# Kernel tuning notes

Measured on AMD Instinct MI355X. Metric: run time of the kernel, lower is better.

The kernel has to match this reference:

```python
import jax, jax.numpy as jnp
import numpy as np

N, E, H = 50000, 800000, 128
EPS = 1e-5

def _init(key, shape, fan_in):
    return jax.random.normal(key, shape, dtype=jnp.float32) / np.sqrt(fan_in)

def setup_inputs() -> dict:
    key = jax.random.key(0)
    ks = jax.random.split(key, 20)
    x = jax.random.normal(ks[0], (N, 3), dtype=jnp.float32)
    h = jax.random.normal(ks[1], (N, H), dtype=jnp.float32)
    edge_index = jax.random.randint(ks[2], (2, E), 0, N, dtype=jnp.int32)
    d_ei = 2 * H + 1
    return {
        "x": x, "h": h, "edge_index": edge_index,
        "We1": _init(ks[3], (d_ei, H), d_ei), "be1": jnp.zeros((H,), jnp.float32),
        "We2": _init(ks[4], (H, H), H),       "be2": jnp.zeros((H,), jnp.float32),
        "Wc1": _init(ks[5], (H, H), H),       "bc1": jnp.zeros((H,), jnp.float32),
        "Wc2": _init(ks[6], (H, 1), H),       "bc2": jnp.zeros((1,), jnp.float32),
        "Wn1": _init(ks[7], (2 * H, H), 2 * H), "bn1": jnp.zeros((H,), jnp.float32),
        "Wn2": _init(ks[8], (H, H), H),       "bn2": jnp.zeros((H,), jnp.float32),
        "gamma": jnp.ones((H,), jnp.float32), "beta": jnp.zeros((H,), jnp.float32),
    }

def reference(x, h, edge_index, We1, be1, We2, be2, Wc1, bc1, Wc2, bc2,
              Wn1, bn1, Wn2, bn2, gamma, beta):
    act = jax.nn.silu
    row, col = edge_index[0], edge_index[1]
    n = x.shape[0]
    rel = x[row] - x[col]                                  # [E,3]
    dist2 = jnp.sum(rel * rel, axis=-1, keepdims=True)     # [E,1]
    edge_input = jnp.concatenate([h[row], h[col], dist2], axis=-1)  # [E,2H+1]
    ef = act(edge_input @ We1 + be1)
    ef = act(ef @ We2 + be2)                                # [E,H]
    gate = act(ef @ Wc1 + bc1) @ Wc2 + bc2                  # [E,1]
    # scatter-mean by row (shared counts for coords and features)
    counts = jax.ops.segment_sum(jnp.ones((rel.shape[0], 1), x.dtype), row, num_segments=n)
    counts = jnp.clip(counts, 1.0)
    dx = jax.ops.segment_sum(rel * gate, row, num_segments=n) / counts
    x_out = x + dx
    agg = jax.ops.segment_sum(ef, row, num_segments=n) / counts     # [N,H]
    dh = act(jnp.concatenate([h, agg], axis=-1) @ Wn1 + bn1) @ Wn2 + bn2
    h2 = h + dh
    mu = jnp.mean(h2, axis=-1, keepdims=True)
    var = jnp.mean((h2 - mu) ** 2, axis=-1, keepdims=True)
    h_norm = (h2 - mu) / jnp.sqrt(var + EPS) * gamma + beta
    h_out = act(h_norm)
    return x_out, h_out
```

## Files before the change

kernel.cpp:

```cpp
#include <hip/hip_runtime.h>

#define NN 50000
#define NE 800000
#define HD 128

typedef __attribute__((ext_vector_type(4))) float vf32x4;
typedef __attribute__((ext_vector_type(8))) __bf16 vbf16x8;
typedef __attribute__((ext_vector_type(4))) unsigned short vushort4;
typedef __attribute__((ext_vector_type(8))) unsigned short vushort8;

constexpr size_t OFF_AGG   = 0;
constexpr size_t OFF_DX    = 25600000;
constexpr size_t OFF_HIST  = 26200000;
constexpr size_t OFF_CUR   = 26400000;
constexpr size_t ZBYTES    = 26600000;
constexpr size_t OFF_START = 26600000;
constexpr size_t OFF_PERM  = 26800704;
constexpr size_t OFF_HBF   = 30000704;
constexpr size_t OFF_HR    = 42800704;
constexpr size_t OFF_HC    = 55600704;
constexpr size_t OFF_WE1P  = 68400704;
constexpr size_t OFF_WE2P  = OFF_WE1P + 65536;
constexpr size_t OFF_WC1P  = OFF_WE2P + 32768;
constexpr size_t OFF_WN1P  = OFF_WC1P + 32768;
constexpr size_t OFF_WN2P  = OFF_WN1P + 65536;

__device__ __forceinline__ unsigned short f2bf(float f) {
    unsigned int u = __float_as_uint(f);
    u += 0x7fffu + ((u >> 16) & 1u);
    return (unsigned short)(u >> 16);
}

__device__ __forceinline__ float bf2f(unsigned short b) {
    return __uint_as_float((unsigned int)b << 16);
}

__device__ __forceinline__ float silu(float v) {
    return __fdividef(v, 1.0f + __expf(-v));
}

__global__ __launch_bounds__(256) void h2bf_kernel(const float* __restrict__ h,
                                                   unsigned short* __restrict__ h_bf) {
    int idx = blockIdx.x * 256 + threadIdx.x;
    vf32x4 v = ((const vf32x4*)h)[idx];
    vushort4 o;
    o[0] = f2bf(v[0]); o[1] = f2bf(v[1]); o[2] = f2bf(v[2]); o[3] = f2bf(v[3]);
    ((vushort4*)h_bf)[idx] = o;
}

__device__ __forceinline__ void pack_one(const float* __restrict__ src,
                                         unsigned short* __restrict__ dst,
                                         int local, int KB) {
    int j = local & 7;
    int lane = (local >> 3) & 63;
    int rest = local >> 9;
    int kb = rest % KB;
    int t = rest / KB;
    int srow = kb * 32 + ((lane >> 4) << 3) + j;
    int scol = t * 16 + (lane & 15);
    dst[local] = f2bf(src[srow * 128 + scol]);
}

__global__ __launch_bounds__(256) void pack_w_kernel(
    const float* __restrict__ We1, const float* __restrict__ We2,
    const float* __restrict__ Wc1, const float* __restrict__ Wn1,
    const float* __restrict__ Wn2,
    unsigned short* __restrict__ We1p, unsigned short* __restrict__ We2p,
    unsigned short* __restrict__ Wc1p, unsigned short* __restrict__ Wn1p,
    unsigned short* __restrict__ Wn2p) {
    int idx = blockIdx.x * 256 + threadIdx.x;
    if (idx < 32768)       pack_one(We1, We1p, idx, 8);
    else if (idx < 49152)  pack_one(We2, We2p, idx - 32768, 4);
    else if (idx < 65536)  pack_one(Wc1, Wc1p, idx - 49152, 4);
    else if (idx < 98304)  pack_one(Wn1, Wn1p, idx - 65536, 8);
    else                   pack_one(Wn2, Wn2p, idx - 98304, 4);
}

__global__ __launch_bounds__(256) void hist_kernel(const int* __restrict__ ei,
                                                   int* __restrict__ hist) {
    int e = blockIdx.x * 256 + threadIdx.x;
    atomicAdd(&hist[ei[e]], 1);
}

#define SCAN_T 1024
#define SCAN_C 49
__global__ __launch_bounds__(1024) void scan_kernel(const int* __restrict__ hist,
                                                    int* __restrict__ row_start) {
    __shared__ int part[SCAN_T];
    int t = threadIdx.x;
    int base = t * SCAN_C;
    int s = 0;
#pragma unroll
    for (int j = 0; j < SCAN_C; j++) {
        int idx = base + j;
        if (idx < NN) s += hist[idx];
    }
    part[t] = s;
    __syncthreads();
    for (int off = 1; off < SCAN_T; off <<= 1) {
        int v = (t >= off) ? part[t - off] : 0;
        __syncthreads();
        part[t] += v;
        __syncthreads();
    }
    int run = (t == 0) ? 0 : part[t - 1];
    for (int j = 0; j < SCAN_C; j++) {
        int idx = base + j;
        if (idx < NN) {
            row_start[idx] = run;
            run += hist[idx];
        }
    }
}

__global__ __launch_bounds__(256) void scatter_kernel(const int* __restrict__ ei,
                                                      const int* __restrict__ row_start,
                                                      int* __restrict__ cursor,
                                                      int* __restrict__ perm) {
    int e = blockIdx.x * 256 + threadIdx.x;
    int r = ei[e];
    int pos = row_start[r] + atomicAdd(&cursor[r], 1);
    perm[pos] = e;
}

__global__ __launch_bounds__(256, 4) void hprep_kernel(
    const unsigned short* __restrict__ h_bf,
    const unsigned short* __restrict__ We1p,
    unsigned short* __restrict__ hr, unsigned short* __restrict__ hc) {
    const int tid = threadIdx.x;
    const int nbase = blockIdx.x * 64;
    const int wave = tid >> 6, lane = tid & 63;
    const int li = lane & 15, grp = lane >> 4;

    int mynode = nbase + wave * 16 + li;
    if (mynode >= NN) mynode = NN - 1;

    vbf16x8 af[4];
    const unsigned short* ph = h_bf + (size_t)mynode * 128 + grp * 8;
#pragma unroll
    for (int kb = 0; kb < 4; kb++) af[kb] = *(const vbf16x8*)(ph + kb * 32);

    const vf32x4 vzero = {0.f, 0.f, 0.f, 0.f};
    vf32x4 ar[8], ac[8];
#pragma unroll
    for (int t = 0; t < 8; t++) { ar[t] = vzero; ac[t] = vzero; }
#pragma unroll
    for (int kb = 0; kb < 4; kb++) {
#pragma unroll
        for (int t = 0; t < 8; t++) {
            vbf16x8 br = *(const vbf16x8*)(We1p + ((t * 8 + kb) * 64 + lane) * 8);
            ar[t] = __builtin_amdgcn_mfma_f32_16x16x32_bf16(af[kb], br, ar[t], 0, 0, 0);
            vbf16x8 bc_ = *(const vbf16x8*)(We1p + ((t * 8 + 4 + kb) * 64 + lane) * 8);
            ac[t] = __builtin_amdgcn_mfma_f32_16x16x32_bf16(af[kb], bc_, ac[t], 0, 0, 0);
        }
    }
#pragma unroll
    for (int t = 0; t < 8; t++) {
        int col = t * 16 + li;
#pragma unroll
        for (int r = 0; r < 4; r++) {
            int node = nbase + wave * 16 + grp * 4 + r;
            if (node < NN) {
                hr[(size_t)node * 128 + col] = f2bf(ar[t][r]);
                hc[(size_t)node * 128 + col] = f2bf(ac[t][r]);
            }
        }
    }
}

__global__ __launch_bounds__(256, 4) void edge_kernel(
    const float* __restrict__ x, const int* __restrict__ ei,
    const int* __restrict__ perm,
    const unsigned short* __restrict__ hr, const unsigned short* __restrict__ hc,
    const unsigned short* __restrict__ We2p, const unsigned short* __restrict__ Wc1p,
    const float* __restrict__ We1, const float* __restrict__ be1,
    const float* __restrict__ be2, const float* __restrict__ bc1,
    const float* __restrict__ Wc2, const float* __restrict__ bc2,
    float* __restrict__ dxsum, float* __restrict__ agg) {

    __shared__ __align__(16) unsigned short s_ef[64 * 136];
    __shared__ float s_rel[64 * 4];
    __shared__ int s_row[64];
    __shared__ int s_col[64];

    const int tid = threadIdx.x;
    const int ebase = blockIdx.x * 64;

    if (tid < 64) {
        int e = perm[ebase + tid];
        int r = ei[e], c = ei[NE + e];
        s_row[tid] = r;
        s_col[tid] = c;
        float d0 = x[r * 3 + 0] - x[c * 3 + 0];
        float d1 = x[r * 3 + 1] - x[c * 3 + 1];
        float d2v = x[r * 3 + 2] - x[c * 3 + 2];
        s_rel[tid * 4 + 0] = d0;
        s_rel[tid * 4 + 1] = d1;
        s_rel[tid * 4 + 2] = d2v;
        s_rel[tid * 4 + 3] = d0 * d0 + d1 * d1 + d2v * d2v;
    }
    __syncthreads();

    const int wave = tid >> 6, lane = tid & 63;
    const int li = lane & 15, grp = lane >> 4;
    const int el = wave * 16 + li;
    const vf32x4 vzero = {0.f, 0.f, 0.f, 0.f};

    vbf16x8 af[4];
    {
        const unsigned short* pr = hr + (size_t)s_row[el] * 128 + grp * 8;
        const unsigned short* pc = hc + (size_t)s_col[el] * 128 + grp * 8;
        const float d2e = s_rel[el * 4 + 3];
        const float* wlast = We1 + 256 * 128;
#pragma unroll
        for (int kb = 0; kb < 4; kb++) {
            vushort8 ua = *(const vushort8*)(pr + kb * 32);
            vushort8 ub = *(const vushort8*)(pc + kb * 32);
            int cbase = kb * 32 + grp * 8;
            vushort8 o;
#pragma unroll
            for (int j = 0; j < 8; j++) {
                float v = bf2f(ua[j]) + bf2f(ub[j]) + d2e * wlast[cbase + j] + be1[cbase + j];
                o[j] = f2bf(silu(v));
            }
            af[kb] = *(vbf16x8*)&o;
        }
    }

    vf32x4 acc[8];
#pragma unroll
    for (int t = 0; t < 8; t++) acc[t] = vzero;
#pragma unroll
    for (int kb = 0; kb < 4; kb++) {
#pragma unroll
        for (int t = 0; t < 8; t++) {
            vbf16x8 b = *(const vbf16x8*)(We2p + ((t * 4 + kb) * 64 + lane) * 8);
            acc[t] = __builtin_amdgcn_mfma_f32_16x16x32_bf16(af[kb], b, acc[t], 0, 0, 0);
        }
    }
#pragma unroll
    for (int t = 0; t < 8; t++) {
        int col = t * 16 + li;
        float b2 = be2[col];
#pragma unroll
        for (int r = 0; r < 4; r++)
            s_ef[(wave * 16 + grp * 4 + r) * 136 + col] = f2bf(silu(acc[t][r] + b2));
    }
    __syncthreads();

#pragma unroll
    for (int t = 0; t < 8; t++) acc[t] = vzero;
    {
        const unsigned short* arow = s_ef + (wave * 16 + li) * 136 + grp * 8;
#pragma unroll
        for (int kb = 0; kb < 4; kb++) {
            vbf16x8 a = *(const vbf16x8*)(arow + kb * 32);
#pragma unroll
            for (int t = 0; t < 8; t++) {
                vbf16x8 b = *(const vbf16x8*)(Wc1p + ((t * 4 + kb) * 64 + lane) * 8);
                acc[t] = __builtin_amdgcn_mfma_f32_16x16x32_bf16(a, b, acc[t], 0, 0, 0);
            }
        }
    }
    float gp[4] = {0.f, 0.f, 0.f, 0.f};
#pragma unroll
    for (int t = 0; t < 8; t++) {
        int col = t * 16 + li;
        float bc = bc1[col], w2 = Wc2[col];
#pragma unroll
        for (int r = 0; r < 4; r++) gp[r] += silu(acc[t][r] + bc) * w2;
    }
#pragma unroll
    for (int r = 0; r < 4; r++) {
#pragma unroll
        for (int d = 1; d < 16; d <<= 1) gp[r] += __shfl_xor(gp[r], d, 16);
        gp[r] += bc2[0];
    }

#pragma unroll
    for (int r = 0; r < 4; r++) {
        int e2 = wave * 16 + grp * 4 + r;
        int node = s_row[e2];
        if (li < 3)
            atomicAdd(&dxsum[node * 3 + li], s_rel[e2 * 4 + li] * gp[r]);
    }

    {
        int col = tid & 127;
        int half = tid >> 7;
        int ebeg = half * 32;
        float acc2 = 0.f;
        int cur = s_row[ebeg];
#pragma unroll 4
        for (int e = ebeg; e < ebeg + 32; ++e) {
            int rr = s_row[e];
            float v = bf2f(s_ef[e * 136 + col]);
            if (rr != cur) {
                atomicAdd(&agg[(size_t)cur * 128 + col], acc2);
                acc2 = 0.f;
                cur = rr;
            }
            acc2 += v;
        }
        atomicAdd(&agg[(size_t)cur * 128 + col], acc2);
    }
}

__global__ __launch_bounds__(256, 4) void node_kernel(
    const float* __restrict__ x, const float* __restrict__ h32,
    const unsigned short* __restrict__ h_bf,
    const int* __restrict__ hist, const float* __restrict__ dxsum,
    const float* __restrict__ agg,
    const unsigned short* __restrict__ Wn1p, const unsigned short* __restrict__ Wn2p,
    const float* __restrict__ bn1, const float* __restrict__ bn2,
    const float* __restrict__ gamma, const float* __restrict__ beta,
    float* __restrict__ out) {

    __shared__ __align__(16) unsigned short s_agg[64 * 136];
    __shared__ __align__(16) unsigned short s_ef[64 * 136];

    const int tid = threadIdx.x;
    const int nbase = blockIdx.x * 64;

    {
        int idx = blockIdx.x * 192 + tid;
        if (tid < 192 && idx < NN * 3) {
            int node = idx / 3;
            float cnt = fmaxf((float)hist[node], 1.0f);
            out[idx] = x[idx] + dxsum[idx] / cnt;
        }
    }
#pragma unroll
    for (int i = 0; i < 8; i++) {
        int flat = i * 256 + tid;
        int row = flat >> 5, q = flat & 31;
        int node = nbase + row;
        if (node >= NN) node = NN - 1;
        float inv = 1.0f / fmaxf((float)hist[node], 1.0f);
        vf32x4 v = *(const vf32x4*)(agg + (size_t)node * 128 + q * 4);
        vushort4 o;
        o[0] = f2bf(v[0] * inv); o[1] = f2bf(v[1] * inv);
        o[2] = f2bf(v[2] * inv); o[3] = f2bf(v[3] * inv);
        *(vushort4*)(&s_agg[row * 136 + q * 4]) = o;
    }
    __syncthreads();

    const int wave = tid >> 6, lane = tid & 63;
    const int li = lane & 15, grp = lane >> 4;
    const vf32x4 vzero = {0.f, 0.f, 0.f, 0.f};

    int mynode = nbase + wave * 16 + li;
    if (mynode >= NN) mynode = NN - 1;

    vbf16x8 af[8];
    {
        const unsigned short* ph = h_bf + (size_t)mynode * 128 + grp * 8;
#pragma unroll
        for (int kb = 0; kb < 4; kb++) af[kb] = *(const vbf16x8*)(ph + kb * 32);
        const unsigned short* pa = s_agg + (wave * 16 + li) * 136 + grp * 8;
#pragma unroll
        for (int kb = 0; kb < 4; kb++) af[4 + kb] = *(const vbf16x8*)(pa + kb * 32);
    }
    vf32x4 acc[8];
#pragma unroll
    for (int t = 0; t < 8; t++) acc[t] = vzero;
#pragma unroll
    for (int kb = 0; kb < 8; kb++) {
#pragma unroll
        for (int t = 0; t < 8; t++) {
            vbf16x8 b = *(const vbf16x8*)(Wn1p + ((t * 8 + kb) * 64 + lane) * 8);
            acc[t] = __builtin_amdgcn_mfma_f32_16x16x32_bf16(af[kb], b, acc[t], 0, 0, 0);
        }
    }
#pragma unroll
    for (int t = 0; t < 8; t++) {
        int col = t * 16 + li;
        float b1 = bn1[col];
#pragma unroll
        for (int r = 0; r < 4; r++) {
            float v = silu(acc[t][r] + b1);
            s_ef[(wave * 16 + grp * 4 + r) * 136 + col] = f2bf(v);
        }
    }
    __syncthreads();

#pragma unroll
    for (int t = 0; t < 8; t++) acc[t] = vzero;
    {
        const unsigned short* arow = s_ef + (wave * 16 + li) * 136 + grp * 8;
#pragma unroll
        for (int kb = 0; kb < 4; kb++) {
            vbf16x8 a = *(const vbf16x8*)(arow + kb * 32);
#pragma unroll
            for (int t = 0; t < 8; t++) {
                vbf16x8 b = *(const vbf16x8*)(Wn2p + ((t * 4 + kb) * 64 + lane) * 8);
                acc[t] = __builtin_amdgcn_mfma_f32_16x16x32_bf16(a, b, acc[t], 0, 0, 0);
            }
        }
    }
    float h2v[8][4];
    float sum[4] = {0.f, 0.f, 0.f, 0.f}, sq[4] = {0.f, 0.f, 0.f, 0.f};
#pragma unroll
    for (int t = 0; t < 8; t++) {
        int col = t * 16 + li;
        float b2 = bn2[col];
#pragma unroll
        for (int r = 0; r < 4; r++) {
            int node = nbase + wave * 16 + grp * 4 + r;
            int nc = node < NN ? node : NN - 1;
            float v = acc[t][r] + b2 + h32[(size_t)nc * 128 + col];
            h2v[t][r] = v;
            sum[r] += v;
            sq[r] += v * v;
        }
    }
    float mu[4], rstd[4];
#pragma unroll
    for (int r = 0; r < 4; r++) {
#pragma unroll
        for (int d = 1; d < 16; d <<= 1) {
            sum[r] += __shfl_xor(sum[r], d, 16);
            sq[r] += __shfl_xor(sq[r], d, 16);
        }
        mu[r] = sum[r] * (1.0f / 128.0f);
        float var = sq[r] * (1.0f / 128.0f) - mu[r] * mu[r];
        rstd[r] = rsqrtf(var + 1e-5f);
    }
#pragma unroll
    for (int t = 0; t < 8; t++) {
        int col = t * 16 + li;
        float g = gamma[col], bt = beta[col];
#pragma unroll
        for (int r = 0; r < 4; r++) {
            int node = nbase + wave * 16 + grp * 4 + r;
            if (node < NN) {
                float vn = (h2v[t][r] - mu[r]) * rstd[r] * g + bt;
                out[NN * 3 + (size_t)node * 128 + col] = silu(vn);
            }
        }
    }
}

extern "C" void kernel_launch(void* const* d_in, const int* in_sizes, int n_in,
                              void* d_out, int out_size, void* d_ws, size_t ws_size,
                              hipStream_t stream) {
    const float* x     = (const float*)d_in[0];
    const float* h     = (const float*)d_in[1];
    const int* ei      = (const int*)d_in[2];
    const float* We1   = (const float*)d_in[3];
    const float* be1   = (const float*)d_in[4];
    const float* We2   = (const float*)d_in[5];
    const float* be2   = (const float*)d_in[6];
    const float* Wc1   = (const float*)d_in[7];
    const float* bc1   = (const float*)d_in[8];
    const float* Wc2   = (const float*)d_in[9];
    const float* bc2   = (const float*)d_in[10];
    const float* Wn1   = (const float*)d_in[11];
    const float* bn1   = (const float*)d_in[12];
    const float* Wn2   = (const float*)d_in[13];
    const float* bn2   = (const float*)d_in[14];
    const float* gamma = (const float*)d_in[15];
    const float* beta  = (const float*)d_in[16];
    float* out = (float*)d_out;

    char* ws = (char*)d_ws;
    float* agg            = (float*)(ws + OFF_AGG);
    float* dxsum          = (float*)(ws + OFF_DX);
    int* hist             = (int*)(ws + OFF_HIST);
    int* cursor           = (int*)(ws + OFF_CUR);
    int* row_start        = (int*)(ws + OFF_START);
    int* perm             = (int*)(ws + OFF_PERM);
    unsigned short* h_bf  = (unsigned short*)(ws + OFF_HBF);
    unsigned short* hr_bf = (unsigned short*)(ws + OFF_HR);
    unsigned short* hc_bf = (unsigned short*)(ws + OFF_HC);
    unsigned short* We1p  = (unsigned short*)(ws + OFF_WE1P);
    unsigned short* We2p  = (unsigned short*)(ws + OFF_WE2P);
    unsigned short* Wc1p  = (unsigned short*)(ws + OFF_WC1P);
    unsigned short* Wn1p  = (unsigned short*)(ws + OFF_WN1P);
    unsigned short* Wn2p  = (unsigned short*)(ws + OFF_WN2P);

    hipMemsetAsync(ws, 0, ZBYTES, stream);
    h2bf_kernel<<<NN * 128 / 4 / 256, 256, 0, stream>>>(h, h_bf);
    pack_w_kernel<<<114688 / 256, 256, 0, stream>>>(We1, We2, Wc1, Wn1, Wn2,
                                                    We1p, We2p, Wc1p, Wn1p, Wn2p);
    hist_kernel<<<NE / 256, 256, 0, stream>>>(ei, hist);
    scan_kernel<<<1, SCAN_T, 0, stream>>>(hist, row_start);
    scatter_kernel<<<NE / 256, 256, 0, stream>>>(ei, row_start, cursor, perm);
    hprep_kernel<<<(NN + 63) / 64, 256, 0, stream>>>(h_bf, We1p, hr_bf, hc_bf);
    edge_kernel<<<NE / 64, 256, 0, stream>>>(x, ei, perm, hr_bf, hc_bf, We2p, Wc1p,
                                             We1, be1, be2, bc1, Wc2, bc2,
                                             dxsum, agg);
    node_kernel<<<(NN + 63) / 64, 256, 0, stream>>>(x, h, h_bf, hist, dxsum, agg,
                                                    Wn1p, Wn2p, bn1, bn2, gamma, beta, out);
}
```

Before: 607.6 us.

## Parallelize row scan, fuse bf16 conversion into hprep, tune edge kernel

Replaces the single-block serial prefix scan with a three-kernel multi-block scan (block sums, scan of sums, local scan plus offset). Folds the h to bf16 conversion into hprep so one kernel launch and a pass over h disappear. In the edge kernel it caches the last We1 row and be1 in shared memory, raises the launch-bounds occupancy hint to 8 blocks per SM, and changes the segmented aggregation to two columns per thread over 16-edge chunks. The higher occupancy hint may force register spills, and the shorter chunks may issue more atomics.

```diff
diff --git a/kernel.cpp b/kernel.cpp
--- a/kernel.cpp
+++ b/kernel.cpp
@@ -24,6 +24,10 @@
 constexpr size_t OFF_WC1P  = OFF_WE2P + 32768;
 constexpr size_t OFF_WN1P  = OFF_WC1P + 32768;
 constexpr size_t OFF_WN2P  = OFF_WN1P + 65536;
+constexpr size_t OFF_BS    = OFF_WN2P + 32768;
+constexpr size_t OFF_BO    = OFF_BS + 1024;
+
+#define NB_SCAN 196
 
 __device__ __forceinline__ unsigned short f2bf(float f) {
     unsigned int u = __float_as_uint(f);
@@ -37,15 +41,6 @@
 
 __device__ __forceinline__ float silu(float v) {
     return __fdividef(v, 1.0f + __expf(-v));
-}
-
-__global__ __launch_bounds__(256) void h2bf_kernel(const float* __restrict__ h,
-                                                   unsigned short* __restrict__ h_bf) {
-    int idx = blockIdx.x * 256 + threadIdx.x;
-    vf32x4 v = ((const vf32x4*)h)[idx];
-    vushort4 o;
-    o[0] = f2bf(v[0]); o[1] = f2bf(v[1]); o[2] = f2bf(v[2]); o[3] = f2bf(v[3]);
-    ((vushort4*)h_bf)[idx] = o;
 }
 
 __device__ __forceinline__ void pack_one(const float* __restrict__ src,
@@ -82,35 +77,51 @@
     atomicAdd(&hist[ei[e]], 1);
 }
 
-#define SCAN_T 1024
-#define SCAN_C 49
-__global__ __launch_bounds__(1024) void scan_kernel(const int* __restrict__ hist,
+__global__ __launch_bounds__(256) void scanA_kernel(const int* __restrict__ hist,
+                                                    int* __restrict__ blocksum) {
+    __shared__ int sm[256];
+    int i = blockIdx.x * 256 + threadIdx.x;
+    sm[threadIdx.x] = (i < NN) ? hist[i] : 0;
+    __syncthreads();
+    for (int off = 128; off > 0; off >>= 1) {
+        if (threadIdx.x < off) sm[threadIdx.x] += sm[threadIdx.x + off];
+        __syncthreads();
+    }
+    if (threadIdx.x == 0) blocksum[blockIdx.x] = sm[0];
+}
+
+__global__ __launch_bounds__(256) void scanB_kernel(const int* __restrict__ blocksum,
+                                                    int* __restrict__ blockoff) {
+    __shared__ int sm[256];
+    int t = threadIdx.x;
+    int v = (t < NB_SCAN) ? blocksum[t] : 0;
+    sm[t] = v;
+    __syncthreads();
+    for (int off = 1; off < 256; off <<= 1) {
+        int u = (t >= off) ? sm[t - off] : 0;
+        __syncthreads();
+        sm[t] += u;
+        __syncthreads();
+    }
+    if (t < NB_SCAN) blockoff[t] = sm[t] - v;
+}
+
+__global__ __launch_bounds__(256) void scanC_kernel(const int* __restrict__ hist,
+                                                    const int* __restrict__ blockoff,
                                                     int* __restrict__ row_start) {
-    __shared__ int part[SCAN_T];
+    __shared__ int sm[256];
+    int i = blockIdx.x * 256 + threadIdx.x;
     int t = threadIdx.x;
-    int base = t * SCAN_C;
-    int s = 0;
-#pragma unroll
-    for (int j = 0; j < SCAN_C; j++) {
-        int idx = base + j;
-        if (idx < NN) s += hist[idx];
-    }
-    part[t] = s;
-    __syncthreads();
-    for (int off = 1; off < SCAN_T; off <<= 1) {
-        int v = (t >= off) ? part[t - off] : 0;
+    int v = (i < NN) ? hist[i] : 0;
+    sm[t] = v;
+    __syncthreads();
+    for (int off = 1; off < 256; off <<= 1) {
+        int u = (t >= off) ? sm[t - off] : 0;
         __syncthreads();
-        part[t] += v;
+        sm[t] += u;
         __syncthreads();
     }
-    int run = (t == 0) ? 0 : part[t - 1];
-    for (int j = 0; j < SCAN_C; j++) {
-        int idx = base + j;
-        if (idx < NN) {
-            row_start[idx] = run;
-            run += hist[idx];
-        }
-    }
+    if (i < NN) row_start[i] = blockoff[blockIdx.x] + sm[t] - v;
 }
 
 __global__ __launch_bounds__(256) void scatter_kernel(const int* __restrict__ ei,
@@ -124,8 +135,9 @@
 }
 
 __global__ __launch_bounds__(256, 4) void hprep_kernel(
-    const unsigned short* __restrict__ h_bf,
+    const float* __restrict__ h,
     const unsigned short* __restrict__ We1p,
+    unsigned short* __restrict__ h_bf,
     unsigned short* __restrict__ hr, unsigned short* __restrict__ hc) {
     const int tid = threadIdx.x;
     const int nbase = blockIdx.x * 64;
@@ -136,9 +148,18 @@
     if (mynode >= NN) mynode = NN - 1;
 
     vbf16x8 af[4];
-    const unsigned short* ph = h_bf + (size_t)mynode * 128 + grp * 8;
-#pragma unroll
-    for (int kb = 0; kb < 4; kb++) af[kb] = *(const vbf16x8*)(ph + kb * 32);
+    const float* ph = h + (size_t)mynode * 128 + grp * 8;
+    unsigned short* pb = h_bf + (size_t)mynode * 128 + grp * 8;
+#pragma unroll
+    for (int kb = 0; kb < 4; kb++) {
+        vf32x4 lo = *(const vf32x4*)(ph + kb * 32);
+        vf32x4 hi = *(const vf32x4*)(ph + kb * 32 + 4);
+        vushort8 o;
+        o[0] = f2bf(lo[0]); o[1] = f2bf(lo[1]); o[2] = f2bf(lo[2]); o[3] = f2bf(lo[3]);
+        o[4] = f2bf(hi[0]); o[5] = f2bf(hi[1]); o[6] = f2bf(hi[2]); o[7] = f2bf(hi[3]);
+        *(vushort8*)(pb + kb * 32) = o;
+        af[kb] = *(vbf16x8*)&o;
+    }
 
     const vf32x4 vzero = {0.f, 0.f, 0.f, 0.f};
     vf32x4 ar[8], ac[8];
@@ -168,7 +189,7 @@
     }
 }
 
-__global__ __launch_bounds__(256, 4) void edge_kernel(
+__global__ __launch_bounds__(256, 8) void edge_kernel(
     const float* __restrict__ x, const int* __restrict__ ei,
     const int* __restrict__ perm,
     const unsigned short* __restrict__ hr, const unsigned short* __restrict__ hc,
@@ -180,6 +201,8 @@
 
     __shared__ __align__(16) unsigned short s_ef[64 * 136];
     __shared__ float s_rel[64 * 4];
+    __shared__ float s_wl[128];
+    __shared__ float s_b1[128];
     __shared__ int s_row[64];
     __shared__ int s_col[64];
 
@@ -199,6 +222,8 @@
         s_rel[tid * 4 + 2] = d2v;
         s_rel[tid * 4 + 3] = d0 * d0 + d1 * d1 + d2v * d2v;
     }
+    if (tid < 128) s_wl[tid] = We1[256 * 128 + tid];
+    else           s_b1[tid - 128] = be1[tid - 128];
     __syncthreads();
 
     const int wave = tid >> 6, lane = tid & 63;
@@ -211,7 +236,6 @@
         const unsigned short* pr = hr + (size_t)s_row[el] * 128 + grp * 8;
         const unsigned short* pc = hc + (size_t)s_col[el] * 128 + grp * 8;
         const float d2e = s_rel[el * 4 + 3];
-        const float* wlast = We1 + 256 * 128;
 #pragma unroll
         for (int kb = 0; kb < 4; kb++) {
             vushort8 ua = *(const vushort8*)(pr + kb * 32);
@@ -220,7 +244,7 @@
             vushort8 o;
 #pragma unroll
             for (int j = 0; j < 8; j++) {
-                float v = bf2f(ua[j]) + bf2f(ub[j]) + d2e * wlast[cbase + j] + be1[cbase + j];
+                float v = bf2f(ua[j]) + bf2f(ub[j]) + d2e * s_wl[cbase + j] + s_b1[cbase + j];
                 o[j] = f2bf(silu(v));
             }
             af[kb] = *(vbf16x8*)&o;
@@ -286,23 +310,27 @@
     }
 
     {
-        int col = tid & 127;
-        int half = tid >> 7;
-        int ebeg = half * 32;
-        float acc2 = 0.f;
+        int p = tid & 63;
+        int q = tid >> 6;
+        int ebeg = q * 16;
+        float a0 = 0.f, a1 = 0.f;
         int cur = s_row[ebeg];
 #pragma unroll 4
-        for (int e = ebeg; e < ebeg + 32; ++e) {
+        for (int e = ebeg; e < ebeg + 16; ++e) {
             int rr = s_row[e];
-            float v = bf2f(s_ef[e * 136 + col]);
+            unsigned int u = *(const unsigned int*)(s_ef + e * 136 + p * 2);
+            float v0 = bf2f((unsigned short)(u & 0xffffu));
+            float v1 = bf2f((unsigned short)(u >> 16));
             if (rr != cur) {
-                atomicAdd(&agg[(size_t)cur * 128 + col], acc2);
-                acc2 = 0.f;
+                atomicAdd(&agg[(size_t)cur * 128 + p * 2], a0);
+                atomicAdd(&agg[(size_t)cur * 128 + p * 2 + 1], a1);
+                a0 = 0.f; a1 = 0.f;
                 cur = rr;
             }
-            acc2 += v;
-        }
-        atomicAdd(&agg[(size_t)cur * 128 + col], acc2);
+            a0 += v0; a1 += v1;
+        }
+        atomicAdd(&agg[(size_t)cur * 128 + p * 2], a0);
+        atomicAdd(&agg[(size_t)cur * 128 + p * 2 + 1], a1);
     }
 }
 
@@ -478,15 +506,18 @@
     unsigned short* Wc1p  = (unsigned short*)(ws + OFF_WC1P);
     unsigned short* Wn1p  = (unsigned short*)(ws + OFF_WN1P);
     unsigned short* Wn2p  = (unsigned short*)(ws + OFF_WN2P);
+    int* blocksum         = (int*)(ws + OFF_BS);
+    int* blockoff         = (int*)(ws + OFF_BO);
 
     hipMemsetAsync(ws, 0, ZBYTES, stream);
-    h2bf_kernel<<<NN * 128 / 4 / 256, 256, 0, stream>>>(h, h_bf);
     pack_w_kernel<<<114688 / 256, 256, 0, stream>>>(We1, We2, Wc1, Wn1, Wn2,
                                                     We1p, We2p, Wc1p, Wn1p, Wn2p);
     hist_kernel<<<NE / 256, 256, 0, stream>>>(ei, hist);
-    scan_kernel<<<1, SCAN_T, 0, stream>>>(hist, row_start);
+    scanA_kernel<<<NB_SCAN, 256, 0, stream>>>(hist, blocksum);
+    scanB_kernel<<<1, 256, 0, stream>>>(blocksum, blockoff);
+    scanC_kernel<<<NB_SCAN, 256, 0, stream>>>(hist, blockoff, row_start);
     scatter_kernel<<<NE / 256, 256, 0, stream>>>(ei, row_start, cursor, perm);
-    hprep_kernel<<<(NN + 63) / 64, 256, 0, stream>>>(h_bf, We1p, hr_bf, hc_bf);
+    hprep_kernel<<<(NN + 63) / 64, 256, 0, stream>>>(h, We1p, h_bf, hr_bf, hc_bf);
     edge_kernel<<<NE / 64, 256, 0, stream>>>(x, ei, perm, hr_bf, hc_bf, We2p, Wc1p,
                                              We1, be1, be2, bc1, Wc2, bc2,
                                              dxsum, agg);
```

After: 496.2 us. 1.22x faster.
